# Performance work log

Measured on AMD Instinct MI355X. Metric: run time of the kernel, lower is better.

The kernel has to match this reference:

```python
import jax, jax.numpy as jnp
import numpy as np

K = 20
EPS = 1e-5
NEG_SLOPE = 0.2


def knn_idx(feat, k):
    # feat: (B, N, C). Pairwise neg squared distance, top-k nearest (self included).
    inner = jnp.einsum('bnc,bmc->bnm', feat, feat)          # (B,N,N)
    sq = jnp.sum(feat * feat, axis=-1)                      # (B,N)
    pd = 2.0 * inner - sq[:, :, None] - sq[:, None, :]      # -||xi-xj||^2
    return jax.lax.top_k(pd, k)[1]                          # (B,N,k)


def edge_conv(feat, W, g, b, m, v, k):
    # feat: (B,N,C); W: (O, 2C); BN params over O channels (eval-mode BN).
    idx = knn_idx(feat, k)                                  # (B,N,k)
    nbr = jnp.take_along_axis(feat[:, None, :, :], idx[..., None], axis=2)  # (B,N,k,C)
    ctr = jnp.broadcast_to(feat[:, :, None, :], nbr.shape)
    edge = jnp.concatenate([nbr - ctr, ctr], axis=-1)       # (B,N,k,2C)
    h = jnp.einsum('bnkc,oc->bnko', edge, W)                # 1x1 conv
    h = (h - m) * (g / jnp.sqrt(v + EPS)) + b               # BatchNorm2d (eval)
    h = jnp.where(h >= 0, h, NEG_SLOPE * h)                 # LeakyReLU(0.2)
    return jnp.max(h, axis=2)                               # max over k -> (B,N,O)


def setup_inputs() -> dict:
    key = jax.random.key(0)
    ks = jax.random.split(key, 21)
    B, N, C = 4, 4096, 3
    d = {'x': jax.random.normal(ks[0], (B, N, C), dtype=jnp.float32)}
    dims = [(64, 2 * 3), (64, 2 * 64), (128, 2 * 64), (256, 2 * 128)]
    for i, (o, c) in enumerate(dims, start=1):
        j = 1 + (i - 1) * 5
        d[f'W{i}'] = jax.random.normal(ks[j], (o, c), dtype=jnp.float32) * (1.0 / np.sqrt(c))
        d[f'g{i}'] = jax.random.uniform(ks[j + 1], (o,), minval=0.5, maxval=1.5, dtype=jnp.float32)
        d[f'b{i}'] = jax.random.normal(ks[j + 2], (o,), dtype=jnp.float32) * 0.1
        d[f'm{i}'] = jax.random.normal(ks[j + 3], (o,), dtype=jnp.float32) * 0.1
        d[f'v{i}'] = jax.random.uniform(ks[j + 4], (o,), minval=0.5, maxval=1.5, dtype=jnp.float32)
    return d


def reference(x, W1, g1, b1, m1, v1, W2, g2, b2, m2, v2,
              W3, g3, b3, m3, v3, W4, g4, b4, m4, v4):
    x1 = edge_conv(x, W1, g1, b1, m1, v1, K)    # (B,N,64)
    x2 = edge_conv(x1, W2, g2, b2, m2, v2, K)   # (B,N,64)
    x3 = edge_conv(x2, W3, g3, b3, m3, v3, K)   # (B,N,128)
    x4 = edge_conv(x3, W4, g4, b4, m4, v4, K)   # (B,N,256)
    return x4
```

## Files before the change

### kernel.cpp

```cpp
#include <hip/hip_runtime.h>

#define NTOT 4096
#define NBATCH 4
#define KNN 20
#define JSPLIT 8
#define KMRG 24
#define CSLOTM 512

constexpr float NEG_INF = -3.0e38f;

typedef __attribute__((ext_vector_type(8))) short bf16x8;
typedef __attribute__((ext_vector_type(4))) float f32x4;

__device__ __forceinline__ unsigned pk(float f, int j) {
  unsigned u = __float_as_uint(f);
  u = (u & 0x80000000u) ? ~u : (u | 0x80000000u);
  return (u & 0xFFFFF000u) | (unsigned)j;
}

__device__ __forceinline__ void pins8(unsigned u, unsigned (&tv)[8]) {
  if (u > tv[0]) {
    tv[0] = u;
#pragma unroll
    for (int x = 1; x < 8; x++) {
      unsigned mn = min(tv[0], tv[x]);
      unsigned mx = max(tv[0], tv[x]);
      tv[0] = mn;
      tv[x] = mx;
    }
  }
}

__device__ __forceinline__ void sbf16(float x, ushort& h16, ushort& l16) {
  unsigned u = __float_as_uint(x);
  unsigned h = (u + 0x7FFFu + ((u >> 16) & 1u)) >> 16;
  float hf = __uint_as_float(h << 16);
  float r = x - hf;
  unsigned v = __float_as_uint(r);
  unsigned l = (v + 0x7FFFu + ((v >> 16) & 1u)) >> 16;
  h16 = (ushort)h;
  l16 = (ushort)l;
}

__device__ __forceinline__ void gll16(const void* g, void* l) {
  __builtin_amdgcn_global_load_lds(
      (const __attribute__((address_space(1))) unsigned int*)g,
      (__attribute__((address_space(3))) unsigned int*)l, 16, 0, 0);
}

__global__ void prep_w(const float* __restrict__ W, const float* __restrict__ gg,
                       const float* __restrict__ bb, const float* __restrict__ mm,
                       const float* __restrict__ vv, float* __restrict__ Wc,
                       float* __restrict__ bias, int O, int C) {
  int t = blockIdx.x * 256 + threadIdx.x;
  if (t >= 2 * O * C) return;
  int o2 = t / C, c = t - o2 * C;
  int o = (o2 < O) ? o2 : o2 - O;
  float s = gg[o] * rsqrtf(vv[o] + 1e-5f);
  float w = (o2 < O) ? W[o * 2 * C + c] * s
                     : (W[o * 2 * C + C + c] - W[o * 2 * C + c]) * s;
  Wc[o2 * C + c] = w;
  if (o2 >= O && c == 0) bias[o] = bb[o] - mm[o] * s;
}

__global__ void cvt3_k(const float* __restrict__ f, ushort* __restrict__ hi,
                       ushort* __restrict__ lo) {
  int p = blockIdx.x * 256 + threadIdx.x;
  int pt = p >> 5, dim = p & 31;
  float x = (dim < 3) ? f[pt * 3 + dim] : 0.f;
  ushort h16, l16;
  sbf16(x, h16, l16);
  hi[p] = h16;
  lo[p] = l16;
}

__global__ void sqh3_k(const float* __restrict__ f, float* __restrict__ sqh) {
  int p = blockIdx.x * 256 + threadIdx.x;
  float a = f[(size_t)p * 3 + 0];
  float b2 = f[(size_t)p * 3 + 1];
  float c = f[(size_t)p * 3 + 2];
  sqh[p] = 0.5f * (a * a + b2 * b2 + c * c);
}

template <int C>
__global__ __launch_bounds__(512, 4) void knn_m(const ushort* __restrict__ Xhi,
                                                const ushort* __restrict__ Xlo,
                                                const float* __restrict__ sqh,
                                                unsigned* __restrict__ cval) {
  constexpr int NK = C / 32;
  constexpr int NJT = NTOT / (128 * JSPLIT);
  constexpr int NSQ = 2 * NJT;
  __shared__ __align__(16) char smem[69632];
  float* sqB = (float*)(smem + 65536);

  int tid = threadIdx.x;
  int raw = blockIdx.x;
  int b = raw & 3;
  int jsp = (raw >> 3) & 3;
  int it = (((raw >> 5) & 15) << 1) | ((raw >> 2) & 1);
  int i0 = it * 128;
  int jpbase = jsp * 1024;
  const ushort* xh = Xhi + (size_t)b * NTOT * C;
  const ushort* xl = Xlo + (size_t)b * NTOT * C;

  int l = tid & 63, wid = tid >> 6;
  int wi = wid & 3, wj = wid >> 2;
  int n = l & 15, quad = l >> 4;
  int xr16 = (n & 7) << 4;

  int t0 = l & 1, t1 = (l >> 1) & 1, t2 = (l >> 2) & 1, t3 = (l >> 3) & 1,
      t4 = (l >> 4) & 1, t5 = (l >> 5) & 1;
  int Rl = (t2 ^ t4) | (t3 << 1) | (t4 << 2) | (t5 << 3);
  int ql = (t0 ^ t2 ^ t4) | ((t1 ^ t3) << 1);

  if (tid < 256) {
    float4 s4 = *(const float4*)&sqh[b * NTOT + jpbase + tid * 4];
    *(float4*)&sqB[tid * 4] = s4;
  }
  __syncthreads();

  unsigned tv[2][8];
#pragma unroll
  for (int ti = 0; ti < 2; ti++)
#pragma unroll
    for (int x = 0; x < 8; x++) tv[ti][x] = 0u;

  auto issue = [&](int sn, int kcn, char* buf) {
    int j0n = jpbase + sn * 128;
    int R = Rl + wid * 16;
    size_t gA = (size_t)(i0 + R) * C + kcn + ql * 8;
    size_t gB = (size_t)(j0n + R) * C + kcn + ql * 8;
    char* ld = buf + wid * 1024;
    gll16(xh + gA, ld);
    gll16(xl + gA, ld + 8192);
    gll16(xh + gB, ld + 16384);
    gll16(xl + gB, ld + 24576);
  };

  issue(0, 0, smem);

  int g = 0;
  for (int s = 0; s < NSQ; s++) {
    int j0 = jpbase + s * 128;

    f32x4 acc[4][2];
#pragma unroll
    for (int tj = 0; tj < 4; tj++)
#pragma unroll
      for (int ti = 0; ti < 2; ti++) acc[tj][ti] = (f32x4)(0.f);

    for (int kc = 0; kc < NK; kc++) {
      __builtin_amdgcn_s_barrier();
      int nsn = (kc + 1 < NK) ? s : ((s + 1 == NSQ) ? 0 : s + 1);
      int nkc = (kc + 1 < NK) ? (kc + 1) * 32 : 0;
      issue(nsn, nkc, smem + ((g + 1) & 1) * 32768);
      asm volatile("s_waitcnt vmcnt(4)" ::: "memory");
      __builtin_amdgcn_s_barrier();
      const char* bc = smem + (g & 1) * 32768;

      bf16x8 ah[2], al_[2];
#pragma unroll
      for (int ti = 0; ti < 2; ti++) {
        int row = wi * 32 + ti * 16 + n;
        int off = (row * 64 + quad * 16) ^ xr16;
        ah[ti] = *(const bf16x8*)(bc + off);
        al_[ti] = *(const bf16x8*)(bc + 8192 + off);
      }
#pragma unroll
      for (int tj = 0; tj < 4; tj++) {
        int row = wj * 64 + tj * 16 + n;
        int off = (row * 64 + quad * 16) ^ xr16;
        bf16x8 bh = *(const bf16x8*)(bc + 16384 + off);
        bf16x8 bl = *(const bf16x8*)(bc + 24576 + off);
#pragma unroll
        for (int ti = 0; ti < 2; ti++) {
          acc[tj][ti] = __builtin_amdgcn_mfma_f32_16x16x32_bf16(bh, ah[ti], acc[tj][ti], 0, 0, 0);
          acc[tj][ti] = __builtin_amdgcn_mfma_f32_16x16x32_bf16(bh, al_[ti], acc[tj][ti], 0, 0, 0);
          acc[tj][ti] = __builtin_amdgcn_mfma_f32_16x16x32_bf16(bl, ah[ti], acc[tj][ti], 0, 0, 0);
        }
      }
      g++;
    }

    float4 sq4[4];
#pragma unroll
    for (int tj = 0; tj < 4; tj++)
      sq4[tj] = *(const float4*)&sqB[s * 128 + wj * 64 + tj * 16 + quad * 4];
#pragma unroll
    for (int ti = 0; ti < 2; ti++) {
#pragma unroll
      for (int tj = 0; tj < 4; tj++) {
        float v0 = acc[tj][ti][0] - sq4[tj].x;
        float v1 = acc[tj][ti][1] - sq4[tj].y;
        float v2 = acc[tj][ti][2] - sq4[tj].z;
        float v3 = acc[tj][ti][3] - sq4[tj].w;
        float m4 = fmaxf(fmaxf(v0, v1), fmaxf(v2, v3));
        if (pk(m4, 0xFFF) > tv[ti][0]) {
          int jb = j0 + wj * 64 + tj * 16 + quad * 4;
          pins8(pk(v0, jb + 0), tv[ti]);
          pins8(pk(v1, jb + 1), tv[ti]);
          pins8(pk(v2, jb + 2), tv[ti]);
          pins8(pk(v3, jb + 3), tv[ti]);
        }
      }
    }

    if (s == NJT - 1 || s == NSQ - 1) {
      int js = jsp * 2 + ((s == NSQ - 1) ? 1 : 0);
#pragma unroll
      for (int ti = 0; ti < 2; ti++) {
        int p = b * NTOT + i0 + wi * 32 + ti * 16 + n;
        unsigned* dst = cval + (size_t)p * CSLOTM + js * 64 + wj * 32 + quad * 8;
        uint4 o0, o1;
        o0.x = tv[ti][0]; o0.y = tv[ti][1]; o0.z = tv[ti][2]; o0.w = tv[ti][3];
        o1.x = tv[ti][4]; o1.y = tv[ti][5]; o1.z = tv[ti][6]; o1.w = tv[ti][7];
        *(uint4*)&dst[0] = o0;
        *(uint4*)&dst[4] = o1;
#pragma unroll
        for (int x = 0; x < 8; x++) tv[ti][x] = 0u;
      }
    }
  }
}

template <int C, int NC>
__global__ __launch_bounds__(256) void kref_w(const float* __restrict__ feat,
                                              const unsigned* __restrict__ cval,
                                              int* __restrict__ outidx) {
  int tid = threadIdx.x;
  int lane = tid & 63;
  int p = blockIdx.x * 4 + (tid >> 6);
  int b = p >> 12;
  int i = p & (NTOT - 1);
  const float* fb = feat + (size_t)b * NTOT * C;

  unsigned c[8];
  {
    uint4 aa = *(const uint4*)&cval[(size_t)p * NC + lane * 8];
    uint4 bb2 = *(const uint4*)&cval[(size_t)p * NC + lane * 8 + 4];
    c[0] = aa.x; c[1] = aa.y; c[2] = aa.z; c[3] = aa.w;
    c[4] = bb2.x; c[5] = bb2.y; c[6] = bb2.z; c[7] = bb2.w;
  }

#define CE(a, bq)                      \
  {                                    \
    unsigned mx = max(c[a], c[bq]);    \
    unsigned mn = min(c[a], c[bq]);    \
    c[a] = mx;                         \
    c[bq] = mn;                        \
  }
  CE(0, 1) CE(2, 3) CE(4, 5) CE(6, 7)
  CE(0, 2) CE(1, 3) CE(4, 6) CE(5, 7)
  CE(1, 2) CE(5, 6) CE(0, 4) CE(3, 7)
  CE(1, 5) CE(2, 6)
  CE(1, 4) CE(3, 6)
  CE(2, 4) CE(3, 5)
  CE(3, 4)
#undef CE

  int myj = -1;
#pragma unroll
  for (int t = 0; t < KMRG; t++) {
    unsigned m = c[0];
#pragma unroll
    for (int s = 1; s < 64; s <<= 1) m = max(m, (unsigned)__shfl_xor((int)m, s));
    if (lane == t) myj = (int)(m & 0xFFFu);
    bool mine = (c[0] == m);
    c[0] = mine ? c[1] : c[0];
    c[1] = mine ? c[2] : c[1];
    c[2] = mine ? c[3] : c[2];
    c[3] = mine ? c[4] : c[3];
    c[4] = mine ? c[5] : c[4];
    c[5] = mine ? c[6] : c[5];
    c[6] = mine ? c[7] : c[6];
    c[7] = mine ? 0u : c[7];
  }

  float myval = NEG_INF;
  if constexpr (C == 3) {
    if (lane < KMRG) {
      float x0 = fb[(size_t)i * 3 + 0];
      float x1 = fb[(size_t)i * 3 + 1];
      float x2 = fb[(size_t)i * 3 + 2];
      float y0 = fb[(size_t)myj * 3 + 0];
      float y1 = fb[(size_t)myj * 3 + 1];
      float y2 = fb[(size_t)myj * 3 + 2];
      float d0 = x0 - y0, d1 = x1 - y1, d2 = x2 - y2;
      myval = -(d0 * d0 + d1 * d1 + d2 * d2);
    }
  } else {
    constexpr int SL = C / 8;
    int m8 = lane & 7;
    float4 xs[SL / 4];
#pragma unroll
    for (int q4 = 0; q4 < SL / 4; q4++)
      xs[q4] = *(const float4*)&fb[(size_t)i * C + m8 * SL + q4 * 4];
#pragma unroll
    for (int ps = 0; ps < KMRG / 8; ps++) {
      int src = ps * 8 + (lane >> 3);
      int j = __shfl(myj, src);
      float d = 0.f;
#pragma unroll
      for (int q4 = 0; q4 < SL / 4; q4++) {
        float4 yv = *(const float4*)&fb[(size_t)j * C + m8 * SL + q4 * 4];
        float dx = xs[q4].x - yv.x;
        float dy = xs[q4].y - yv.y;
        float dz = xs[q4].z - yv.z;
        float dw = xs[q4].w - yv.w;
        d += dx * dx + dy * dy + dz * dz + dw * dw;
      }
#pragma unroll
      for (int s = 1; s < 8; s <<= 1) d += __shfl_xor(d, s);
      float sd = __shfl(d, (lane & 7) << 3);
      bool upd = ((lane >> 3) == ps);
      myval = upd ? -sd : myval;
    }
  }

#pragma unroll
  for (int k = 2; k <= 64; k <<= 1) {
#pragma unroll
    for (int j2 = k >> 1; j2 > 0; j2 >>= 1) {
      float ov = __shfl_xor(myval, j2);
      int oj = __shfl_xor(myj, j2);
      bool ogt = (ov > myval) || (ov == myval && oj < myj);
      bool lower = ((lane & j2) == 0);
      bool desc = ((lane & k) == 0);
      bool take = (desc == (lower == ogt));
      myval = take ? ov : myval;
      myj = take ? oj : myj;
    }
  }

  if (lane < KNN) outidx[(size_t)p * KNN + lane] = myj;
}

__global__ __launch_bounds__(256) void gemm128(const float* __restrict__ A,
                                               const float* __restrict__ Wc,
                                               const float* __restrict__ bias,
                                               float* __restrict__ Y, int K, int N2,
                                               int O) {
  constexpr int P = 140;
  __shared__ float As[16 * P];
  __shared__ float Bs[16 * P];
  int tid = threadIdx.x;
  int n0 = blockIdx.x * 128;
  int m0 = blockIdx.y * 128;
  int tx = tid & 15, ty = tid >> 4;
  int aoff = (ty * 8) + (((ty * 8) >> 5) << 2);
  int boff = (tx * 8) + (((tx * 8) >> 5) << 2);
  float acc[8][8];
#pragma unroll
  for (int ii = 0; ii < 8; ii++)
#pragma unroll
    for (int jj = 0; jj < 8; jj++) acc[ii][jj] = 0.f;

  for (int kc = 0; kc < K; kc += 16) {
    __syncthreads();
#pragma unroll
    for (int l = 0; l < 2; l++) {
      int e = tid + 256 * l;
      int rr = e >> 2, c4 = e & 3;
      int sc = rr + ((rr >> 5) << 2);
      float4 va = *(const float4*)&A[(size_t)(m0 + rr) * K + kc + c4 * 4];
      As[(c4 * 4 + 0) * P + sc] = va.x;
      As[(c4 * 4 + 1) * P + sc] = va.y;
      As[(c4 * 4 + 2) * P + sc] = va.z;
      As[(c4 * 4 + 3) * P + sc] = va.w;
      float4 vb = *(const float4*)&Wc[(size_t)(n0 + rr) * K + kc + c4 * 4];
      Bs[(c4 * 4 + 0) * P + sc] = vb.x;
      Bs[(c4 * 4 + 1) * P + sc] = vb.y;
      Bs[(c4 * 4 + 2) * P + sc] = vb.z;
      Bs[(c4 * 4 + 3) * P + sc] = vb.w;
    }
    __syncthreads();
#pragma unroll 8
    for (int k = 0; k < 16; k++) {
      float4 a0 = *(const float4*)&As[k * P + aoff];
      float4 a1 = *(const float4*)&As[k * P + aoff + 4];
      float4 b0 = *(const float4*)&Bs[k * P + boff];
      float4 b1 = *(const float4*)&Bs[k * P + boff + 4];
      float av[8] = {a0.x, a0.y, a0.z, a0.w, a1.x, a1.y, a1.z, a1.w};
      float bv[8] = {b0.x, b0.y, b0.z, b0.w, b1.x, b1.y, b1.z, b1.w};
#pragma unroll
      for (int ii = 0; ii < 8; ii++)
#pragma unroll
        for (int jj = 0; jj < 8; jj++)
          acc[ii][jj] = fmaf(av[ii], bv[jj], acc[ii][jj]);
    }
  }

  int col0 = n0 + tx * 8;
  float bv[8];
#pragma unroll
  for (int jj = 0; jj < 8; jj++) {
    int col = col0 + jj;
    bv[jj] = (col >= O) ? bias[col - O] : 0.f;
  }
#pragma unroll
  for (int ii = 0; ii < 8; ii++) {
    int row = m0 + ty * 8 + ii;
    float4 o0, o1;
    o0.x = acc[ii][0] + bv[0];
    o0.y = acc[ii][1] + bv[1];
    o0.z = acc[ii][2] + bv[2];
    o0.w = acc[ii][3] + bv[3];
    o1.x = acc[ii][4] + bv[4];
    o1.y = acc[ii][5] + bv[5];
    o1.z = acc[ii][6] + bv[6];
    o1.w = acc[ii][7] + bv[7];
    *(float4*)&Y[(size_t)row * N2 + col0] = o0;
    *(float4*)&Y[(size_t)row * N2 + col0 + 4] = o1;
  }
}

__global__ __launch_bounds__(256) void gemm_k(const float* __restrict__ A,
                                              const float* __restrict__ Wc,
                                              const float* __restrict__ bias,
                                              float* __restrict__ Y, int K, int N2,
                                              int O) {
  __shared__ float As[8 * 68];
  __shared__ float Bs[8 * 68];
  int tid = threadIdx.x;
  int n0 = blockIdx.x * 64;
  int m0 = blockIdx.y * 64;
  int tx = tid & 15, ty = tid >> 4;
  float acc[4][4] = {};
  for (int k0 = 0; k0 < K; k0 += 8) {
    __syncthreads();
    {
      int e = tid, mm = e >> 3, kk = e & 7;
      As[kk * 68 + mm] = (k0 + kk < K) ? A[(size_t)(m0 + mm) * K + k0 + kk] : 0.f;
      int nn = mm;
      Bs[kk * 68 + nn] = (k0 + kk < K) ? Wc[(size_t)(n0 + nn) * K + k0 + kk] : 0.f;
      e = tid + 256;
      mm = e >> 3;
      kk = e & 7;
      As[kk * 68 + mm] = (k0 + kk < K) ? A[(size_t)(m0 + mm) * K + k0 + kk] : 0.f;
      nn = mm;
      Bs[kk * 68 + nn] = (k0 + kk < K) ? Wc[(size_t)(n0 + nn) * K + k0 + kk] : 0.f;
    }
    __syncthreads();
#pragma unroll
    for (int kk = 0; kk < 8; kk++) {
      float4 av = *(float4*)&As[kk * 68 + ty * 4];
      float4 bv = *(float4*)&Bs[kk * 68 + tx * 4];
      float a[4] = {av.x, av.y, av.z, av.w};
      float bb2[4] = {bv.x, bv.y, bv.z, bv.w};
#pragma unroll
      for (int ii = 0; ii < 4; ii++)
#pragma unroll
        for (int jj = 0; jj < 4; jj++) acc[ii][jj] += a[ii] * bb2[jj];
    }
  }
  int col = n0 + tx * 4;
  bool isV = (col >= O);
  float b0 = 0.f, b1 = 0.f, b2 = 0.f, b3 = 0.f;
  if (isV) {
    b0 = bias[col + 0 - O];
    b1 = bias[col + 1 - O];
    b2 = bias[col + 2 - O];
    b3 = bias[col + 3 - O];
  }
#pragma unroll
  for (int ii = 0; ii < 4; ii++) {
    int row = m0 + ty * 4 + ii;
    float4 o4;
    o4.x = acc[ii][0] + b0;
    o4.y = acc[ii][1] + b1;
    o4.z = acc[ii][2] + b2;
    o4.w = acc[ii][3] + b3;
    *(float4*)&Y[(size_t)row * N2 + col] = o4;
  }
}

template <int O, int CN>
__global__ __launch_bounds__(256) void gmax_v(const float* __restrict__ Y,
                                              const int* __restrict__ idx,
                                              float* __restrict__ out,
                                              ushort* __restrict__ nxh,
                                              ushort* __restrict__ nxl,
                                              float* __restrict__ nsq) {
  constexpr int T = O / 4;
  constexpr int G = 256 / T;
  int tid = threadIdx.x;
  int p = blockIdx.x * G + tid / T;
  int o4 = (tid % T) * 4;
  int b = p >> 12;
  constexpr int N2 = 2 * O;
  const int* ip = idx + (size_t)p * KNN;
  float4 m = make_float4(NEG_INF, NEG_INF, NEG_INF, NEG_INF);
#pragma unroll
  for (int k = 0; k < KNN; k++) {
    int j = ip[k];
    float4 v = *(const float4*)&Y[((size_t)(b * NTOT + j)) * N2 + o4];
    m.x = fmaxf(m.x, v.x);
    m.y = fmaxf(m.y, v.y);
    m.z = fmaxf(m.z, v.z);
    m.w = fmaxf(m.w, v.w);
  }
  float4 c = *(const float4*)&Y[(size_t)p * N2 + O + o4];
  float4 o;
  o.x = c.x + m.x;
  o.y = c.y + m.y;
  o.z = c.z + m.z;
  o.w = c.w + m.w;
  o.x = (o.x >= 0.f) ? o.x : 0.2f * o.x;
  o.y = (o.y >= 0.f) ? o.y : 0.2f * o.y;
  o.z = (o.z >= 0.f) ? o.z : 0.2f * o.z;
  o.w = (o.w >= 0.f) ? o.w : 0.2f * o.w;
  *(float4*)&out[(size_t)p * O + o4] = o;

  if constexpr (CN != 0) {
    ushort4 h4, l4;
    sbf16(o.x, h4.x, l4.x);
    sbf16(o.y, h4.y, l4.y);
    sbf16(o.z, h4.z, l4.z);
    sbf16(o.w, h4.w, l4.w);
    *(ushort4*)&nxh[(size_t)p * O + o4] = h4;
    *(ushort4*)&nxl[(size_t)p * O + o4] = l4;
    float ss = o.x * o.x + o.y * o.y + o.z * o.z + o.w * o.w;
#pragma unroll
    for (int s = 1; s < T; s <<= 1) ss += __shfl_xor(ss, s);
    if ((tid & (T - 1)) == 0) nsq[p] = 0.5f * ss;
  }
}

template <int C, int O, int CN>
static void run_layer(const float* fin, void* const* w5, float* fout, float* Wc,
                      float* biasb, int* idx, float* Y, float* sqh,
                      unsigned* cval, ushort* Xhi, ushort* Xlo,
                      ushort* nxh, ushort* nxl, hipStream_t stream) {
  const float* W = (const float*)w5[0];
  const float* g = (const float*)w5[1];
  const float* bb = (const float*)w5[2];
  const float* mm = (const float*)w5[3];
  const float* vv = (const float*)w5[4];
  int N2 = 2 * O;
  prep_w<<<(2 * O * C + 255) / 256, 256, 0, stream>>>(W, g, bb, mm, vv, Wc, biasb, O, C);
  if (C == 3) {
    cvt3_k<<<NBATCH * NTOT * 32 / 256, 256, 0, stream>>>(fin, Xhi, Xlo);
    sqh3_k<<<NBATCH * NTOT / 256, 256, 0, stream>>>(fin, sqh);
    knn_m<32><<<NBATCH * 32 * (JSPLIT / 2), 512, 0, stream>>>(Xhi, Xlo, sqh, cval);
    kref_w<3, 512><<<NBATCH * NTOT / 4, 256, 0, stream>>>(fin, cval, idx);
    dim3 gg(N2 / 64, NBATCH * NTOT / 64);
    gemm_k<<<gg, 256, 0, stream>>>(fin, Wc, biasb, Y, C, N2, O);
  } else {
    knn_m<C><<<NBATCH * 32 * (JSPLIT / 2), 512, 0, stream>>>(Xhi, Xlo, sqh, cval);
    kref_w<C, 512><<<NBATCH * NTOT / 4, 256, 0, stream>>>(fin, cval, idx);
    dim3 gg(N2 / 128, NBATCH * NTOT / 128);
    gemm128<<<gg, 256, 0, stream>>>(fin, Wc, biasb, Y, C, N2, O);
  }
  gmax_v<O, CN><<<NBATCH * NTOT / (256 / (O / 4)), 256, 0, stream>>>(
      Y, idx, fout, nxh, nxl, sqh);
}

extern "C" void kernel_launch(void* const* d_in, const int* in_sizes, int n_in,
                              void* d_out, int out_size, void* d_ws, size_t ws_size,
                              hipStream_t stream) {
  const float* x = (const float*)d_in[0];
  char* ws = (char*)d_ws;
  float* Wc = (float*)(ws + 0);
  float* biasb = (float*)(ws + 262144);
  int* idx = (int*)(ws + 263168);
  float* sqh = (float*)(ws + 1573888);
  float* Y = (float*)(ws + 1639424);
  float* x1 = (float*)(ws + 35193856);
  float* x2 = (float*)(ws + 39388160);
  float* x3 = (float*)(ws + 43582464);

  unsigned* cval = (unsigned*)Y;
  ushort* X1h = (ushort*)x1;
  ushort* X1l = X1h + (size_t)NBATCH * NTOT * 32;
  ushort* X2h = (ushort*)x2;
  ushort* X2l = X2h + (size_t)NBATCH * NTOT * 64;
  ushort* X3h = (ushort*)x3;
  ushort* X3l = X3h + (size_t)NBATCH * NTOT * 64;
  float* outf = (float*)d_out;
  ushort* X4h = (ushort*)outf;
  ushort* X4l = X4h + (size_t)NBATCH * NTOT * 128;

  run_layer<3, 64, 64>(x, d_in + 1, x1, Wc, biasb, idx, Y, sqh, cval,
                       X1h, X1l, X2h, X2l, stream);
  run_layer<64, 64, 64>(x1, d_in + 6, x2, Wc, biasb, idx, Y, sqh, cval,
                        X2h, X2l, X3h, X3l, stream);
  run_layer<64, 128, 128>(x2, d_in + 11, x3, Wc, biasb, idx, Y, sqh, cval,
                          X3h, X3l, X4h, X4l, stream);
  run_layer<128, 256, 0>(x3, d_in + 16, outf, Wc, biasb, idx, Y, sqh, cval,
                         X4h, X4l, nullptr, nullptr, stream);
}
```

Baseline: 651.1 us.

## Double KNN block to 16 waves and process two points per wave in refine

The KNN distance kernel now runs 1024 threads per block. Each wave owns a single 16-row i-tile instead of two, and loading is split so half the waves fetch A tiles and half fetch B tiles. Each wave therefore carries less accumulator and top-k register state, which should allow more waves in flight per CU. The refine kernel now has each wave handle two query points, interleaving their shuffle reductions and bitonic sorts to expose ILP and halve the block count. The cost is less LDS fragment reuse per wave and more barrier participants per block.

```diff
diff --git a/kernel.cpp b/kernel.cpp
--- a/kernel.cpp
+++ b/kernel.cpp
@@ -83,10 +83,10 @@
 }
 
 template <int C>
-__global__ __launch_bounds__(512, 4) void knn_m(const ushort* __restrict__ Xhi,
-                                                const ushort* __restrict__ Xlo,
-                                                const float* __restrict__ sqh,
-                                                unsigned* __restrict__ cval) {
+__global__ __launch_bounds__(1024, 8) void knn_m(const ushort* __restrict__ Xhi,
+                                                 const ushort* __restrict__ Xlo,
+                                                 const float* __restrict__ sqh,
+                                                 unsigned* __restrict__ cval) {
   constexpr int NK = C / 32;
   constexpr int NJT = NTOT / (128 * JSPLIT);
   constexpr int NSQ = 2 * NJT;
@@ -104,7 +104,7 @@
   const ushort* xl = Xlo + (size_t)b * NTOT * C;
 
   int l = tid & 63, wid = tid >> 6;
-  int wi = wid & 3, wj = wid >> 2;
+  int wi = wid & 7, wj = wid >> 3;
   int n = l & 15, quad = l >> 4;
   int xr16 = (n & 7) << 4;
 
@@ -119,22 +119,24 @@
   }
   __syncthreads();
 
-  unsigned tv[2][8];
-#pragma unroll
-  for (int ti = 0; ti < 2; ti++)
-#pragma unroll
-    for (int x = 0; x < 8; x++) tv[ti][x] = 0u;
+  unsigned tv[8];
+#pragma unroll
+  for (int x = 0; x < 8; x++) tv[x] = 0u;
 
   auto issue = [&](int sn, int kcn, char* buf) {
-    int j0n = jpbase + sn * 128;
-    int R = Rl + wid * 16;
-    size_t gA = (size_t)(i0 + R) * C + kcn + ql * 8;
-    size_t gB = (size_t)(j0n + R) * C + kcn + ql * 8;
-    char* ld = buf + wid * 1024;
-    gll16(xh + gA, ld);
-    gll16(xl + gA, ld + 8192);
-    gll16(xh + gB, ld + 16384);
-    gll16(xl + gB, ld + 24576);
+    int band = wid & 7;
+    int R = Rl + band * 16;
+    char* ld = buf + band * 1024;
+    if (wid < 8) {
+      size_t gA = (size_t)(i0 + R) * C + kcn + ql * 8;
+      gll16(xh + gA, ld);
+      gll16(xl + gA, ld + 8192);
+    } else {
+      int j0n = jpbase + sn * 128;
+      size_t gB = (size_t)(j0n + R) * C + kcn + ql * 8;
+      gll16(xh + gB, ld + 16384);
+      gll16(xl + gB, ld + 24576);
+    }
   };
 
   issue(0, 0, smem);
@@ -143,41 +145,32 @@
   for (int s = 0; s < NSQ; s++) {
     int j0 = jpbase + s * 128;
 
-    f32x4 acc[4][2];
-#pragma unroll
-    for (int tj = 0; tj < 4; tj++)
-#pragma unroll
-      for (int ti = 0; ti < 2; ti++) acc[tj][ti] = (f32x4)(0.f);
+    f32x4 acc[4];
+#pragma unroll
+    for (int tj = 0; tj < 4; tj++) acc[tj] = (f32x4)(0.f);
 
     for (int kc = 0; kc < NK; kc++) {
       __builtin_amdgcn_s_barrier();
       int nsn = (kc + 1 < NK) ? s : ((s + 1 == NSQ) ? 0 : s + 1);
       int nkc = (kc + 1 < NK) ? (kc + 1) * 32 : 0;
       issue(nsn, nkc, smem + ((g + 1) & 1) * 32768);
-      asm volatile("s_waitcnt vmcnt(4)" ::: "memory");
+      asm volatile("s_waitcnt vmcnt(2)" ::: "memory");
       __builtin_amdgcn_s_barrier();
       const char* bc = smem + (g & 1) * 32768;
 
-      bf16x8 ah[2], al_[2];
-#pragma unroll
-      for (int ti = 0; ti < 2; ti++) {
-        int row = wi * 32 + ti * 16 + n;
-        int off = (row * 64 + quad * 16) ^ xr16;
-        ah[ti] = *(const bf16x8*)(bc + off);
-        al_[ti] = *(const bf16x8*)(bc + 8192 + off);
-      }
+      int arow = wi * 16 + n;
+      int aoff = (arow * 64 + quad * 16) ^ xr16;
+      bf16x8 ah = *(const bf16x8*)(bc + aoff);
+      bf16x8 al_ = *(const bf16x8*)(bc + 8192 + aoff);
 #pragma unroll
       for (int tj = 0; tj < 4; tj++) {
-        int row = wj * 64 + tj * 16 + n;
-        int off = (row * 64 + quad * 16) ^ xr16;
-        bf16x8 bh = *(const bf16x8*)(bc + 16384 + off);
-        bf16x8 bl = *(const bf16x8*)(bc + 24576 + off);
-#pragma unroll
-        for (int ti = 0; ti < 2; ti++) {
-          acc[tj][ti] = __builtin_amdgcn_mfma_f32_16x16x32_bf16(bh, ah[ti], acc[tj][ti], 0, 0, 0);
-          acc[tj][ti] = __builtin_amdgcn_mfma_f32_16x16x32_bf16(bh, al_[ti], acc[tj][ti], 0, 0, 0);
-          acc[tj][ti] = __builtin_amdgcn_mfma_f32_16x16x32_bf16(bl, ah[ti], acc[tj][ti], 0, 0, 0);
-        }
+        int brow = wj * 64 + tj * 16 + n;
+        int boff = (brow * 64 + quad * 16) ^ xr16;
+        bf16x8 bh = *(const bf16x8*)(bc + 16384 + boff);
+        bf16x8 bl = *(const bf16x8*)(bc + 24576 + boff);
+        acc[tj] = __builtin_amdgcn_mfma_f32_16x16x32_bf16(bh, ah, acc[tj], 0, 0, 0);
+        acc[tj] = __builtin_amdgcn_mfma_f32_16x16x32_bf16(bh, al_, acc[tj], 0, 0, 0);
+        acc[tj] = __builtin_amdgcn_mfma_f32_16x16x32_bf16(bl, ah, acc[tj], 0, 0, 0);
       }
       g++;
     }
@@ -187,38 +180,32 @@
     for (int tj = 0; tj < 4; tj++)
       sq4[tj] = *(const float4*)&sqB[s * 128 + wj * 64 + tj * 16 + quad * 4];
 #pragma unroll
-    for (int ti = 0; ti < 2; ti++) {
-#pragma unroll
-      for (int tj = 0; tj < 4; tj++) {
-        float v0 = acc[tj][ti][0] - sq4[tj].x;
-        float v1 = acc[tj][ti][1] - sq4[tj].y;
-        float v2 = acc[tj][ti][2] - sq4[tj].z;
-        float v3 = acc[tj][ti][3] - sq4[tj].w;
-        float m4 = fmaxf(fmaxf(v0, v1), fmaxf(v2, v3));
-        if (pk(m4, 0xFFF) > tv[ti][0]) {
-          int jb = j0 + wj * 64 + tj * 16 + quad * 4;
-          pins8(pk(v0, jb + 0), tv[ti]);
-          pins8(pk(v1, jb + 1), tv[ti]);
-          pins8(pk(v2, jb + 2), tv[ti]);
-          pins8(pk(v3, jb + 3), tv[ti]);
-        }
+    for (int tj = 0; tj < 4; tj++) {
+      float v0 = acc[tj][0] - sq4[tj].x;
+      float v1 = acc[tj][1] - sq4[tj].y;
+      float v2 = acc[tj][2] - sq4[tj].z;
+      float v3 = acc[tj][3] - sq4[tj].w;
+      float m4 = fmaxf(fmaxf(v0, v1), fmaxf(v2, v3));
+      if (pk(m4, 0xFFF) > tv[0]) {
+        int jb = j0 + wj * 64 + tj * 16 + quad * 4;
+        pins8(pk(v0, jb + 0), tv);
+        pins8(pk(v1, jb + 1), tv);
+        pins8(pk(v2, jb + 2), tv);
+        pins8(pk(v3, jb + 3), tv);
       }
     }
 
     if (s == NJT - 1 || s == NSQ - 1) {
       int js = jsp * 2 + ((s == NSQ - 1) ? 1 : 0);
-#pragma unroll
-      for (int ti = 0; ti < 2; ti++) {
-        int p = b * NTOT + i0 + wi * 32 + ti * 16 + n;
-        unsigned* dst = cval + (size_t)p * CSLOTM + js * 64 + wj * 32 + quad * 8;
-        uint4 o0, o1;
-        o0.x = tv[ti][0]; o0.y = tv[ti][1]; o0.z = tv[ti][2]; o0.w = tv[ti][3];
-        o1.x = tv[ti][4]; o1.y = tv[ti][5]; o1.z = tv[ti][6]; o1.w = tv[ti][7];
-        *(uint4*)&dst[0] = o0;
-        *(uint4*)&dst[4] = o1;
-#pragma unroll
-        for (int x = 0; x < 8; x++) tv[ti][x] = 0u;
-      }
+      int p = b * NTOT + i0 + wi * 16 + n;
+      unsigned* dst = cval + (size_t)p * CSLOTM + js * 64 + wj * 32 + quad * 8;
+      uint4 o0, o1;
+      o0.x = tv[0]; o0.y = tv[1]; o0.z = tv[2]; o0.w = tv[3];
+      o1.x = tv[4]; o1.y = tv[5]; o1.z = tv[6]; o1.w = tv[7];
+      *(uint4*)&dst[0] = o0;
+      *(uint4*)&dst[4] = o1;
+#pragma unroll
+      for (int x = 0; x < 8; x++) tv[x] = 0u;
     }
   }
 }
@@ -229,91 +216,111 @@
                                               int* __restrict__ outidx) {
   int tid = threadIdx.x;
   int lane = tid & 63;
-  int p = blockIdx.x * 4 + (tid >> 6);
-  int b = p >> 12;
-  int i = p & (NTOT - 1);
-  const float* fb = feat + (size_t)b * NTOT * C;
-
-  unsigned c[8];
-  {
+  int pbase = blockIdx.x * 8 + (tid >> 6) * 2;
+
+  unsigned c[2][8];
+  int bq[2], iq[2];
+#pragma unroll
+  for (int pt = 0; pt < 2; pt++) {
+    int p = pbase + pt;
+    bq[pt] = p >> 12;
+    iq[pt] = p & (NTOT - 1);
     uint4 aa = *(const uint4*)&cval[(size_t)p * NC + lane * 8];
     uint4 bb2 = *(const uint4*)&cval[(size_t)p * NC + lane * 8 + 4];
-    c[0] = aa.x; c[1] = aa.y; c[2] = aa.z; c[3] = aa.w;
-    c[4] = bb2.x; c[5] = bb2.y; c[6] = bb2.z; c[7] = bb2.w;
-  }
-
-#define CE(a, bq)                      \
-  {                                    \
-    unsigned mx = max(c[a], c[bq]);    \
-    unsigned mn = min(c[a], c[bq]);    \
-    c[a] = mx;                         \
-    c[bq] = mn;                        \
-  }
-  CE(0, 1) CE(2, 3) CE(4, 5) CE(6, 7)
-  CE(0, 2) CE(1, 3) CE(4, 6) CE(5, 7)
-  CE(1, 2) CE(5, 6) CE(0, 4) CE(3, 7)
-  CE(1, 5) CE(2, 6)
-  CE(1, 4) CE(3, 6)
-  CE(2, 4) CE(3, 5)
-  CE(3, 4)
+    c[pt][0] = aa.x; c[pt][1] = aa.y; c[pt][2] = aa.z; c[pt][3] = aa.w;
+    c[pt][4] = bb2.x; c[pt][5] = bb2.y; c[pt][6] = bb2.z; c[pt][7] = bb2.w;
+  }
+
+#define CE(a, bq2)                          \
+  {                                         \
+    unsigned mx = max(c[pt][a], c[pt][bq2]); \
+    unsigned mn = min(c[pt][a], c[pt][bq2]); \
+    c[pt][a] = mx;                          \
+    c[pt][bq2] = mn;                        \
+  }
+#pragma unroll
+  for (int pt = 0; pt < 2; pt++) {
+    CE(0, 1) CE(2, 3) CE(4, 5) CE(6, 7)
+    CE(0, 2) CE(1, 3) CE(4, 6) CE(5, 7)
+    CE(1, 2) CE(5, 6) CE(0, 4) CE(3, 7)
+    CE(1, 5) CE(2, 6)
+    CE(1, 4) CE(3, 6)
+    CE(2, 4) CE(3, 5)
+    CE(3, 4)
+  }
 #undef CE
 
-  int myj = -1;
+  int myj[2] = {-1, -1};
 #pragma unroll
   for (int t = 0; t < KMRG; t++) {
-    unsigned m = c[0];
-#pragma unroll
-    for (int s = 1; s < 64; s <<= 1) m = max(m, (unsigned)__shfl_xor((int)m, s));
-    if (lane == t) myj = (int)(m & 0xFFFu);
-    bool mine = (c[0] == m);
-    c[0] = mine ? c[1] : c[0];
-    c[1] = mine ? c[2] : c[1];
-    c[2] = mine ? c[3] : c[2];
-    c[3] = mine ? c[4] : c[3];
-    c[4] = mine ? c[5] : c[4];
-    c[5] = mine ? c[6] : c[5];
-    c[6] = mine ? c[7] : c[6];
-    c[7] = mine ? 0u : c[7];
-  }
-
-  float myval = NEG_INF;
+#pragma unroll
+    for (int pt = 0; pt < 2; pt++) {
+      unsigned m = c[pt][0];
+#pragma unroll
+      for (int s = 1; s < 64; s <<= 1)
+        m = max(m, (unsigned)__shfl_xor((int)m, s));
+      if (lane == t) myj[pt] = (int)(m & 0xFFFu);
+      bool mine = (c[pt][0] == m);
+      c[pt][0] = mine ? c[pt][1] : c[pt][0];
+      c[pt][1] = mine ? c[pt][2] : c[pt][1];
+      c[pt][2] = mine ? c[pt][3] : c[pt][2];
+      c[pt][3] = mine ? c[pt][4] : c[pt][3];
+      c[pt][4] = mine ? c[pt][5] : c[pt][4];
+      c[pt][5] = mine ? c[pt][6] : c[pt][5];
+      c[pt][6] = mine ? c[pt][7] : c[pt][6];
+      c[pt][7] = mine ? 0u : c[pt][7];
+    }
+  }
+
+  float myval[2] = {NEG_INF, NEG_INF};
   if constexpr (C == 3) {
-    if (lane < KMRG) {
-      float x0 = fb[(size_t)i * 3 + 0];
-      float x1 = fb[(size_t)i * 3 + 1];
-      float x2 = fb[(size_t)i * 3 + 2];
-      float y0 = fb[(size_t)myj * 3 + 0];
-      float y1 = fb[(size_t)myj * 3 + 1];
-      float y2 = fb[(size_t)myj * 3 + 2];
-      float d0 = x0 - y0, d1 = x1 - y1, d2 = x2 - y2;
-      myval = -(d0 * d0 + d1 * d1 + d2 * d2);
+#pragma unroll
+    for (int pt = 0; pt < 2; pt++) {
+      const float* fb = feat + (size_t)bq[pt] * NTOT * 3;
+      if (lane < KMRG) {
+        float x0 = fb[(size_t)iq[pt] * 3 + 0];
+        float x1 = fb[(size_t)iq[pt] * 3 + 1];
+        float x2 = fb[(size_t)iq[pt] * 3 + 2];
+        float y0 = fb[(size_t)myj[pt] * 3 + 0];
+        float y1 = fb[(size_t)myj[pt] * 3 + 1];
+        float y2 = fb[(size_t)myj[pt] * 3 + 2];
+        float d0 = x0 - y0, d1 = x1 - y1, d2 = x2 - y2;
+        myval[pt] = -(d0 * d0 + d1 * d1 + d2 * d2);
+      }
     }
   } else {
     constexpr int SL = C / 8;
     int m8 = lane & 7;
-    float4 xs[SL / 4];
-#pragma unroll
-    for (int q4 = 0; q4 < SL / 4; q4++)
-      xs[q4] = *(const float4*)&fb[(size_t)i * C + m8 * SL + q4 * 4];
+    float4 xs[2][SL / 4];
+#pragma unroll
+    for (int pt = 0; pt < 2; pt++)
+#pragma unroll
+      for (int q4 = 0; q4 < SL / 4; q4++)
+        xs[pt][q4] = *(const float4*)&feat[((size_t)bq[pt] * NTOT + iq[pt]) * C +
+                                           m8 * SL + q4 * 4];
 #pragma unroll
     for (int ps = 0; ps < KMRG / 8; ps++) {
       int src = ps * 8 + (lane >> 3);
-      int j = __shfl(myj, src);
-      float d = 0.f;
-#pragma unroll
-      for (int q4 = 0; q4 < SL / 4; q4++) {
-        float4 yv = *(const float4*)&fb[(size_t)j * C + m8 * SL + q4 * 4];
-        float dx = xs[q4].x - yv.x;
-        float dy = xs[q4].y - yv.y;
-        float dz = xs[q4].z - yv.z;
-        float dw = xs[q4].w - yv.w;
-        d += dx * dx + dy * dy + dz * dz + dw * dw;
+#pragma unroll
+      for (int pt = 0; pt < 2; pt++) {
+        int j = __shfl(myj[pt], src);
+        float d = 0.f;
+#pragma unroll
+        for (int q4 = 0; q4 < SL / 4; q4++) {
+          float4 yv = *(const float4*)&feat[((size_t)bq[pt] * NTOT + j) * C +
+                                            m8 * SL + q4 * 4];
+          float dx = xs[pt][q4].x - yv.x;
+          float dy = xs[pt][q4].y - yv.y;
+          float dz = xs[pt][q4].z - yv.z;
+          float dw = xs[pt][q4].w - yv.w;
+          d += dx * dx + dy * dy + dz * dz + dw * dw;
+        }
+#pragma unroll
+        for (int s = 1; s < 8; s <<= 1) d += __shfl_xor(d, s);
+        float sd = __shfl(d, (lane & 7) << 3);
+        bool upd = ((lane >> 3) == ps);
+        myval[pt] = upd ? -sd : myval[pt];
       }
-#pragma unroll
-      for (int s = 1; s < 8; s <<= 1) d += __shfl_xor(d, s);
-      float sd = __shfl(d, (lane & 7) << 3);
-      bool upd = ((lane >> 3) == ps);
-      myval = upd ? -sd : myval;
     }
   }
 
@@ -321,18 +328,23 @@
   for (int k = 2; k <= 64; k <<= 1) {
 #pragma unroll
     for (int j2 = k >> 1; j2 > 0; j2 >>= 1) {
-      float ov = __shfl_xor(myval, j2);
-      int oj = __shfl_xor(myj, j2);
-      bool ogt = (ov > myval) || (ov == myval && oj < myj);
-      bool lower = ((lane & j2) == 0);
-      bool desc = ((lane & k) == 0);
-      bool take = (desc == (lower == ogt));
-      myval = take ? ov : myval;
-      myj = take ? oj : myj;
-    }
-  }
-
-  if (lane < KNN) outidx[(size_t)p * KNN + lane] = myj;
+#pragma unroll
+      for (int pt = 0; pt < 2; pt++) {
+        float ov = __shfl_xor(myval[pt], j2);
+        int oj = __shfl_xor(myj[pt], j2);
+        bool ogt = (ov > myval[pt]) || (ov == myval[pt] && oj < myj[pt]);
+        bool lower = ((lane & j2) == 0);
+        bool desc = ((lane & k) == 0);
+        bool take = (desc == (lower == ogt));
+        myval[pt] = take ? ov : myval[pt];
+        myj[pt] = take ? oj : myj[pt];
+      }
+    }
+  }
+
+#pragma unroll
+  for (int pt = 0; pt < 2; pt++)
+    if (lane < KNN) outidx[(size_t)(pbase + pt) * KNN + lane] = myj[pt];
 }
 
 __global__ __launch_bounds__(256) void gemm128(const float* __restrict__ A,
@@ -541,13 +553,13 @@
   if (C == 3) {
     cvt3_k<<<NBATCH * NTOT * 32 / 256, 256, 0, stream>>>(fin, Xhi, Xlo);
     sqh3_k<<<NBATCH * NTOT / 256, 256, 0, stream>>>(fin, sqh);
-    knn_m<32><<<NBATCH * 32 * (JSPLIT / 2), 512, 0, stream>>>(Xhi, Xlo, sqh, cval);
-    kref_w<3, 512><<<NBATCH * NTOT / 4, 256, 0, stream>>>(fin, cval, idx);
+    knn_m<32><<<NBATCH * 32 * (JSPLIT / 2), 1024, 0, stream>>>(Xhi, Xlo, sqh, cval);
+    kref_w<3, 512><<<NBATCH * NTOT / 8, 256, 0, stream>>>(fin, cval, idx);
     dim3 gg(N2 / 64, NBATCH * NTOT / 64);
     gemm_k<<<gg, 256, 0, stream>>>(fin, Wc, biasb, Y, C, N2, O);
   } else {
-    knn_m<C><<<NBATCH * 32 * (JSPLIT / 2), 512, 0, stream>>>(Xhi, Xlo, sqh, cval);
-    kref_w<C, 512><<<NBATCH * NTOT / 4, 256, 0, stream>>>(fin, cval, idx);
+    knn_m<C><<<NBATCH * 32 * (JSPLIT / 2), 1024, 0, stream>>>(Xhi, Xlo, sqh, cval);
+    kref_w<C, 512><<<NBATCH * NTOT / 8, 256, 0, stream>>>(fin, cval, idx);
     dim3 gg(N2 / 128, NBATCH * NTOT / 128);
     gemm128<<<gg, 256, 0, stream>>>(fin, Wc, biasb, Y, C, N2, O);
   }
```

Result: slower. 668.7 us (+2.7%).
